# Kernel optimization log

Measured on AMD Instinct MI355X. Metric: run time of the kernel, lower is better.

Reference implementation:

```python
import jax, jax.numpy as jnp
import numpy as np

FEAT_DIM = 32
RES = 256
N_GAUSS = 500000
KSIZE = 5
SIGMA = 1.0


def setup_inputs() -> dict:
    key = jax.random.key(0)
    k0, k1, k2, k3, k4 = jax.random.split(key, 5)
    plane_xy = jax.random.normal(k0, (1, FEAT_DIM, RES, RES), jnp.float32)
    plane_xz = jax.random.normal(k1, (1, FEAT_DIM, RES, RES), jnp.float32)
    plane_yz = jax.random.normal(k2, (1, FEAT_DIM, RES, RES), jnp.float32)
    ln_weight = jnp.ones((FEAT_DIM, RES, RES), jnp.float32)
    ln_bias = jnp.zeros((FEAT_DIM, RES, RES), jnp.float32)
    gaussian_features = jax.random.normal(k3, (N_GAUSS, 3 * FEAT_DIM), jnp.float32)
    gaussian_xyz = jax.random.uniform(k4, (N_GAUSS, 3), jnp.float32, -1.0, 1.0)
    return {"plane_xy": plane_xy, "plane_xz": plane_xz, "plane_yz": plane_yz,
            "ln_weight": ln_weight, "ln_bias": ln_bias,
            "gaussian_features": gaussian_features, "gaussian_xyz": gaussian_xyz}


def _gaussian_blur(x):
    # depthwise 5x5 gaussian blur, groups = channels
    c = x.shape[1]
    k = jnp.arange(-(KSIZE // 2), KSIZE // 2 + 1, dtype=jnp.float32)
    k = jnp.exp(-0.5 * (k / SIGMA) ** 2)
    k = k / k.sum()
    k2d = k[:, None] * k[None, :]                       # [5,5]
    kern = jnp.broadcast_to(k2d, (c, 1, KSIZE, KSIZE))  # OIHW, grouped
    return jax.lax.conv_general_dilated(
        x, kern, window_strides=(1, 1), padding="SAME",
        feature_group_count=c,
        dimension_numbers=("NCHW", "OIHW", "NCHW"))


def _update_plane(plane, idx, feats, ln_w, ln_b):
    # plane [1,C,H,W]; idx [N,2] float pixel coords (x,y); feats [N,C]
    _, C, H, W = plane.shape
    px, py = idx[:, 0], idx[:, 1]
    px0 = jnp.clip(jnp.floor(px).astype(jnp.int32), 0, W - 1)
    px1 = jnp.clip(jnp.floor(px).astype(jnp.int32) + 1, 0, W - 1)
    py0 = jnp.clip(jnp.floor(py).astype(jnp.int32), 0, H - 1)
    py1 = jnp.clip(jnp.floor(py).astype(jnp.int32) + 1, 0, H - 1)
    wx0 = jnp.clip(px1.astype(px.dtype) - px, 0.0, 1.0)
    wx1 = jnp.clip(px - px0.astype(px.dtype), 0.0, 1.0)
    wy0 = jnp.clip(py1.astype(py.dtype) - py, 0.0, 1.0)
    wy1 = jnp.clip(py - py0.astype(py.dtype), 0.0, 1.0)
    weights = jnp.stack([wx0 * wy0, wx0 * wy1, wx1 * wy0, wx1 * wy1], axis=-1)  # [N,4]
    iy = jnp.stack([py0, py1, py0, py1], axis=-1)  # [N,4]
    ix = jnp.stack([px0, px0, px1, px1], axis=-1)  # [N,4]
    lin = (iy * W + ix).reshape(-1)                # [N*4]
    wf = (feats[:, None, :] * weights[:, :, None]).reshape(-1, C)  # [N*4, C]
    acc = jnp.zeros((H * W, C), plane.dtype).at[lin].add(wf)       # scatter-add
    counts = jnp.zeros((H * W,), plane.dtype).at[lin].add(1.0)
    flat = plane.reshape(C, H * W)
    # straight-through: value = scattered features, grad flows identity to plane
    new = flat + jax.lax.stop_gradient(-flat) + acc.T
    new = new / (counts[None, :] + 1e-6)
    new = new.reshape(1, C, H, W)
    # LayerNorm over (C,H,W)
    mu = jnp.mean(new, axis=(1, 2, 3), keepdims=True)
    var = jnp.var(new, axis=(1, 2, 3), keepdims=True)
    new = (new - mu) / jnp.sqrt(var + 1e-5) * ln_w[None] + ln_b[None]
    new = _gaussian_blur(new)
    return new + plane


def reference(plane_xy, plane_xz, plane_yz, ln_weight, ln_bias,
              gaussian_features, gaussian_xyz):
    res = plane_xy.shape[-1]
    xyz01 = (gaussian_xyz + 1.0) / 2.0
    x = jnp.clip(xyz01[..., 0], 0.0, 0.999) * (res - 1)
    y = jnp.clip(xyz01[..., 1], 0.0, 0.999) * (res - 1)
    z = jnp.clip(xyz01[..., 2], 0.0, 0.999) * (res - 1)
    feats = gaussian_features.reshape(gaussian_xyz.shape[0], 3, -1)
    new_xy = _update_plane(plane_xy, jnp.stack([x, y], -1), feats[:, 0, :], ln_weight, ln_bias)
    new_xz = _update_plane(plane_xz, jnp.stack([x, z], -1), feats[:, 1, :], ln_weight, ln_bias)
    new_yz = _update_plane(plane_yz, jnp.stack([y, z], -1), feats[:, 2, :], ln_weight, ln_bias)
    return (new_xy, new_xz, new_yz)
```

## Files before the change

kernel.cpp:

```cpp
#include <hip/hip_runtime.h>
#include <hip/hip_bf16.h>

#define N_GAUSS 500000
#define NGP (N_GAUSS * 3)
#define FEAT 32
#define RES 256
#define HW (RES * RES)
#define PLANE_ELEMS (FEAT * HW)
#define NBINS (3 * HW)

typedef __hip_bfloat16 bf16;

__device__ __forceinline__ bool input_is_bf16(const void* lnw) {
  return ((const unsigned int*)lnw)[0] == 0x3F803F80u;
}

template <bool BF16>
__device__ __forceinline__ float ldin(const void* p, size_t i) {
  if constexpr (BF16)
    return __bfloat162float(((const bf16*)p)[i]);
  else
    return ((const float*)p)[i];
}

template <bool BF16>
__device__ __forceinline__ float2 ldin2(const void* p, size_t i) {
  if constexpr (BF16) {
    unsigned u = *(const unsigned*)((const bf16*)p + i);
    return make_float2(__uint_as_float(u << 16),
                       __uint_as_float(u & 0xFFFF0000u));
  } else {
    return *(const float2*)((const float*)p + i);
  }
}

template <bool BF16>
__device__ __forceinline__ void stout(void* p, size_t i, float v) {
  if constexpr (BF16)
    ((bf16*)p)[i] = __float2bfloat16(v);
  else
    ((float*)p)[i] = v;
}

template <bool BF16>
__device__ __forceinline__ void gpos(const void* xyz, int g, int p, float& px,
                                     float& py) {
  int dx = (p == 2) ? 1 : 0;
  int dy = (p == 0) ? 1 : 2;
  float vx = ldin<BF16>(xyz, 3 * g + dx);
  float vy = ldin<BF16>(xyz, 3 * g + dy);
  px = fminf(fmaxf((vx + 1.0f) * 0.5f, 0.0f), 0.999f) * (float)(RES - 1);
  py = fminf(fmaxf((vy + 1.0f) * 0.5f, 0.0f), 0.999f) * (float)(RES - 1);
}

template <bool BF16>
__device__ __forceinline__ void count_impl(const void* xyz,
                                           int* __restrict__ bincnt) {
  int t = blockIdx.x * 256 + threadIdx.x;
  if (t >= NGP) return;
  int g = t / 3;
  int p = t - g * 3;
  float px, py;
  gpos<BF16>(xyz, g, p, px, py);
  atomicAdd(&bincnt[(p << 16) + ((int)py << 8) + (int)px], 1);
}

__global__ __launch_bounds__(256) void count_kernel(const void* __restrict__ xyz,
                                                    const void* __restrict__ lnw,
                                                    int* __restrict__ bincnt) {
  if (input_is_bf16(lnw))
    count_impl<true>(xyz, bincnt);
  else
    count_impl<false>(xyz, bincnt);
}

__global__ __launch_bounds__(256) void scan1_kernel(const int* __restrict__ bincnt,
                                                    int* __restrict__ off,
                                                    int* __restrict__ bsum) {
  int tid = threadIdx.x;
  int4 v = ((const int4*)bincnt)[blockIdx.x * 256 + tid];
  int s = v.x + v.y + v.z + v.w;
  __shared__ int ls[256];
  ls[tid] = s;
  __syncthreads();
  for (int o = 1; o < 256; o <<= 1) {
    int t = 0;
    if (tid >= o) t = ls[tid - o];
    __syncthreads();
    ls[tid] += t;
    __syncthreads();
  }
  int excl = ls[tid] - s;
  int base = blockIdx.x * 1024 + tid * 4;
  off[base + 0] = excl;
  off[base + 1] = excl + v.x;
  off[base + 2] = excl + v.x + v.y;
  off[base + 3] = excl + v.x + v.y + v.z;
  if (tid == 255) bsum[blockIdx.x] = ls[255];
}

__global__ __launch_bounds__(256) void scan23_kernel(int* __restrict__ off,
                                                     const int* __restrict__ bsum) {
  __shared__ int ls[256];
  __shared__ int ex[192];
  int tid = threadIdx.x;
  int v = (tid < 192) ? bsum[tid] : 0;
  ls[tid] = v;
  __syncthreads();
  for (int o = 1; o < 256; o <<= 1) {
    int t = 0;
    if (tid >= o) t = ls[tid - o];
    __syncthreads();
    ls[tid] += t;
    __syncthreads();
  }
  if (tid < 192) ex[tid] = ls[tid] - v;
  __syncthreads();
  int i = blockIdx.x * 256 + tid;
  off[i] += ex[blockIdx.x >> 2];
}

template <bool BF16>
__device__ __forceinline__ void scatter_impl(const void* xyz,
                                             int* __restrict__ off,
                                             int* __restrict__ entries) {
  int t = blockIdx.x * 256 + threadIdx.x;
  if (t >= NGP) return;
  int g = t / 3;
  int p = t - g * 3;
  float px, py;
  gpos<BF16>(xyz, g, p, px, py);
  int slot = atomicAdd(&off[(p << 16) + ((int)py << 8) + (int)px], 1);
  entries[slot * 3 + 0] = __float_as_int(px);
  entries[slot * 3 + 1] = __float_as_int(py);
  entries[slot * 3 + 2] = t << 5;
}

__global__ __launch_bounds__(256) void scatter_kernel(
    const void* __restrict__ xyz, const void* __restrict__ lnw,
    int* __restrict__ off, int* __restrict__ entries) {
  if (input_is_bf16(lnw))
    scatter_impl<true>(xyz, off, entries);
  else
    scatter_impl<false>(xyz, off, entries);
}

template <bool BF16>
__device__ __forceinline__ void gather_impl(const int* __restrict__ off,
                                            const int* __restrict__ bincnt,
                                            const int* __restrict__ entries,
                                            const void* __restrict__ feats,
                                            float* __restrict__ nb,
                                            float* tile) {
  int wid = threadIdx.x >> 6;
  int lane = threadIdx.x & 63;
  int c = lane & 31;
  int sub = lane >> 5;
  int pid4 = (blockIdx.x * 4 + wid) * 4;
  int p = pid4 >> 16;
  int pix = pid4 & 65535;
  int y = pix >> 8;
  int x0 = pix & 255;
  float fyq = (float)y;
  float fx0f = (float)x0;

  int bxlo = max(x0 - 1, 0);
  int rbA = (p << 16) + ((y - 1) << 8);
  int rbB = (p << 16) + (y << 8);
  int sA = 0, eA = 0;
  if (y > 0) {
    int bA0 = rbA + bxlo;
    sA = off[bA0] - bincnt[bA0];
    eA = off[rbA + x0 + 3];
  }
  int bB0 = rbB + bxlo;
  int sB = off[bB0] - bincnt[bB0];
  int eB = off[rbB + x0 + 3];

  int s0 = 0, s1 = 0, s2 = 0, s3 = 0, s4 = 0;
  {
    int col;
    col = x0 - 1;
    if (col >= 0) {
      s0 = bincnt[rbB + col];
      if (y > 0) s0 += bincnt[rbA + col];
    }
    col = x0;
    s1 = bincnt[rbB + col];
    if (y > 0) s1 += bincnt[rbA + col];
    col = x0 + 1;
    s2 = bincnt[rbB + col];
    if (y > 0) s2 += bincnt[rbA + col];
    col = x0 + 2;
    s3 = bincnt[rbB + col];
    if (y > 0) s3 += bincnt[rbA + col];
    col = x0 + 3;
    s4 = bincnt[rbB + col];
    if (y > 0) s4 += bincnt[rbA + col];
  }
  int cnt0 = s0 + s1, cnt1 = s1 + s2, cnt2 = s2 + s3, cnt3 = s3 + s4;

  float a0 = 0.0f, a1 = 0.0f, a2 = 0.0f, a3 = 0.0f;
#pragma unroll 1
  for (int rr = 0; rr < 2; ++rr) {
    int start = rr ? sB : sA;
    int end = rr ? eB : eA;
#pragma unroll 1
    for (int base = start; base < end; base += 20) {
      int n = end - base;
      n = n > 20 ? 20 : n;
      int d = 0;
      if (lane < n * 3) d = entries[base * 3 + lane];
      int l = lane < 20 ? lane : 19;
      float epx = __int_as_float(__shfl(d, 3 * l + 0));
      float epy = __int_as_float(__shfl(d, 3 * l + 1));
      int fbp = __shfl(d, 3 * l + 2);
      float wy = 1.0f - fabsf(epy - fyq);
      float u = epx - fx0f;
      float w0p = fmaxf(1.0f - fabsf(u), 0.0f) * wy;
      float w1p = fmaxf(1.0f - fabsf(u - 1.0f), 0.0f) * wy;
      float w2p = fmaxf(1.0f - fabsf(u - 2.0f), 0.0f) * wy;
      float w3p = fmaxf(1.0f - fabsf(u - 3.0f), 0.0f) * wy;
#pragma unroll 1
      for (int k = 0; k < n; k += 2) {
        int idx = k + sub;
        int is = idx < n ? idx : 0;
        int fb = __shfl(fbp, is);
        float f = ldin<BF16>(feats, (size_t)fb + c);
        if (idx >= n) f = 0.0f;
        a0 = fmaf(__shfl(w0p, is), f, a0);
        a1 = fmaf(__shfl(w1p, is), f, a1);
        a2 = fmaf(__shfl(w2p, is), f, a2);
        a3 = fmaf(__shfl(w3p, is), f, a3);
      }
    }
  }
  a0 += __shfl_xor(a0, 32);
  a1 += __shfl_xor(a1, 32);
  a2 += __shfl_xor(a2, 32);
  a3 += __shfl_xor(a3, 32);
  if (sub == 0) {
    int lb = (wid << 2);
    tile[c * 17 + lb + 0] = a0 / ((float)cnt0 + 1e-6f);
    tile[c * 17 + lb + 1] = a1 / ((float)cnt1 + 1e-6f);
    tile[c * 17 + lb + 2] = a2 / ((float)cnt2 + 1e-6f);
    tile[c * 17 + lb + 3] = a3 / ((float)cnt3 + 1e-6f);
  }
  __syncthreads();
  int c2 = threadIdx.x >> 4;
  int lp = threadIdx.x & 15;
  int pix0 = (blockIdx.x << 4) & 65535;
  size_t b = ((size_t)p << 21) + pix0 + lp;
  nb[b + ((size_t)c2 << 16)] = tile[c2 * 17 + lp];
  nb[b + ((size_t)(c2 + 16) << 16)] = tile[(c2 + 16) * 17 + lp];
}

__global__ __launch_bounds__(256) void gather_kernel(
    const int* __restrict__ off, const int* __restrict__ bincnt,
    const int* __restrict__ entries, const void* __restrict__ feats,
    const void* __restrict__ lnw, float* __restrict__ nb) {
  __shared__ float tile[32 * 17];
  if (input_is_bf16(lnw))
    gather_impl<true>(off, bincnt, entries, feats, nb, tile);
  else
    gather_impl<false>(off, bincnt, entries, feats, nb, tile);
}

__global__ __launch_bounds__(256) void stats_kernel(const float* __restrict__ nb,
                                                    double* __restrict__ stats) {
  int b = blockIdx.x;
  int p = b >> 8;
  int blk = b & 255;
  const float4* nb4 = (const float4*)(nb + ((size_t)p << 21));
  int tid = threadIdx.x;
  float s = 0.0f, s2 = 0.0f;
#pragma unroll
  for (int k = 0; k < 8; ++k) {
    float4 v = nb4[blk * 2048 + k * 256 + tid];
    s += (v.x + v.y) + (v.z + v.w);
    s2 += (v.x * v.x + v.y * v.y) + (v.z * v.z + v.w * v.w);
  }
  __shared__ float ls[256];
  __shared__ float ls2[256];
  ls[tid] = s;
  ls2[tid] = s2;
  __syncthreads();
  for (int o = 128; o > 0; o >>= 1) {
    if (tid < o) {
      ls[tid] += ls[tid + o];
      ls2[tid] += ls2[tid + o];
    }
    __syncthreads();
  }
  if (tid == 0) {
    unsafeAtomicAdd(&stats[2 * p + 0], (double)ls[0]);
    unsafeAtomicAdd(&stats[2 * p + 1], (double)ls2[0]);
  }
}

template <bool BF16>
__device__ __forceinline__ void blur_impl(const float* __restrict__ nb,
                                          const double* __restrict__ stats,
                                          const void* __restrict__ lnw,
                                          const void* __restrict__ lnb,
                                          const void* __restrict__ pl,
                                          void* __restrict__ out,
                                          float (*sm)[36]) {
  int p = blockIdx.z >> 5;
  int c = blockIdx.z & 31;
  const float* np = nb + ((size_t)p << 21) + ((size_t)c << 16);

  double mu_d = stats[2 * p] * (1.0 / PLANE_ELEMS);
  double var_d = stats[2 * p + 1] * (1.0 / PLANE_ELEMS) - mu_d * mu_d;
  float mu = (float)mu_d;
  float inv = rsqrtf((float)var_d + 1e-5f);

  int tx = threadIdx.x, ty = threadIdx.y;
  int w0 = blockIdx.x * 32, h0 = blockIdx.y * 8;
  int lid = ty * 32 + tx;
  for (int li = lid; li < 12 * 18; li += 256) {
    int r = li / 18;
    int m = li - r * 18;
    int hh = h0 - 2 + r;
    int ww = w0 - 2 + (m << 1);
    float v0 = 0.0f, v1 = 0.0f;
    if ((unsigned)hh < 256u && (unsigned)ww < 256u) {
      int pix = (hh << 8) + ww;
      float2 av = *(const float2*)(np + pix);
      size_t gi = ((size_t)c << 16) + pix;
      float2 lw = ldin2<BF16>(lnw, gi);
      float2 lb = ldin2<BF16>(lnb, gi);
      v0 = (av.x - mu) * inv * lw.x + lb.x;
      v1 = (av.y - mu) * inv * lw.y + lb.y;
    }
    sm[r][(m << 1) + 0] = v0;
    sm[r][(m << 1) + 1] = v1;
  }
  __syncthreads();

  const float K[5] = {0.054488685f, 0.24420134f, 0.40261996f, 0.24420134f,
                      0.054488685f};
  float a = 0.0f;
#pragma unroll
  for (int i = 0; i < 5; i++) {
    float rs = 0.0f;
#pragma unroll
    for (int j = 0; j < 5; j++) rs += K[j] * sm[ty + i][tx + j];
    a += K[i] * rs;
  }
  size_t idx = ((size_t)c << 16) + ((h0 + ty) << 8) + w0 + tx;
  float res = a + ldin<BF16>(pl, idx);
  stout<BF16>(out, ((size_t)p << 21) + idx, res);
}

__global__ __launch_bounds__(256) void blur_kernel(
    const float* __restrict__ nb, const double* __restrict__ stats,
    const void* __restrict__ lnw, const void* __restrict__ lnb,
    const void* __restrict__ p0, const void* __restrict__ p1,
    const void* __restrict__ p2, void* __restrict__ out) {
  __shared__ float sm[12][36];
  int p = blockIdx.z >> 5;
  const void* pl = (p == 0) ? p0 : ((p == 1) ? p1 : p2);
  if (input_is_bf16(lnw))
    blur_impl<true>(nb, stats, lnw, lnb, pl, out, sm);
  else
    blur_impl<false>(nb, stats, lnw, lnb, pl, out, sm);
}

extern "C" void kernel_launch(void* const* d_in, const int* in_sizes, int n_in,
                              void* d_out, int out_size, void* d_ws,
                              size_t ws_size, hipStream_t stream) {
  const void* plane_xy = d_in[0];
  const void* plane_xz = d_in[1];
  const void* plane_yz = d_in[2];
  const void* lnw = d_in[3];
  const void* lnb = d_in[4];
  const void* feats = d_in[5];
  const void* xyz = d_in[6];

  char* ws = (char*)d_ws;
  int* bincnt = (int*)ws;
  double* stats = (double*)(ws + 786432);
  int* off = (int*)(ws + 786480);
  int* bsum = (int*)(ws + 1572912);
  int* entries = (int*)(ws + 1574448);
  float* nb = (float*)(ws + 19574448);

  hipMemsetAsync(d_ws, 0, 786480, stream);

  int gp_blocks = (NGP + 255) / 256;
  count_kernel<<<gp_blocks, 256, 0, stream>>>(xyz, lnw, bincnt);
  scan1_kernel<<<192, 256, 0, stream>>>(bincnt, off, bsum);
  scan23_kernel<<<NBINS / 256, 256, 0, stream>>>(off, bsum);
  scatter_kernel<<<gp_blocks, 256, 0, stream>>>(xyz, lnw, off, entries);
  gather_kernel<<<NBINS / 16, 256, 0, stream>>>(off, bincnt, entries, feats,
                                                lnw, nb);
  stats_kernel<<<768, 256, 0, stream>>>(nb, stats);
  blur_kernel<<<dim3(8, 32, 96), dim3(32, 8), 0, stream>>>(
      nb, stats, lnw, lnb, plane_xy, plane_xz, plane_yz, d_out);
}
```

Measured before the change: 685.9 us.

## Process one gaussian per thread in count/scatter; prefetch entries and unroll gather loop

The count and scatter kernels now handle one gaussian per thread and cover all three planes, loading the xyz coordinates once instead of three times and dropping the divide-by-3. The gather kernel software-prefetches the next batch of 20 entries while it processes the current one, and fully unrolls the inner feature loop to 10 iterations with masking, so more feature loads can be in flight at once. The prefetch reads past the end of a bin's range, possibly past the end of the entries array, and may load garbage or out-of-bounds data. The unrolled loop also does wasted shuffles when a batch holds fewer than 20 entries.

Result: faster. 616.1 us (-10.2%).

```diff
diff --git a/kernel.cpp b/kernel.cpp
--- a/kernel.cpp
+++ b/kernel.cpp
@@ -42,27 +42,22 @@
     ((float*)p)[i] = v;
 }
 
-template <bool BF16>
-__device__ __forceinline__ void gpos(const void* xyz, int g, int p, float& px,
-                                     float& py) {
-  int dx = (p == 2) ? 1 : 0;
-  int dy = (p == 0) ? 1 : 2;
-  float vx = ldin<BF16>(xyz, 3 * g + dx);
-  float vy = ldin<BF16>(xyz, 3 * g + dy);
-  px = fminf(fmaxf((vx + 1.0f) * 0.5f, 0.0f), 0.999f) * (float)(RES - 1);
-  py = fminf(fmaxf((vy + 1.0f) * 0.5f, 0.0f), 0.999f) * (float)(RES - 1);
+__device__ __forceinline__ float gscale(float v) {
+  return fminf(fmaxf((v + 1.0f) * 0.5f, 0.0f), 0.999f) * (float)(RES - 1);
 }
 
 template <bool BF16>
 __device__ __forceinline__ void count_impl(const void* xyz,
                                            int* __restrict__ bincnt) {
-  int t = blockIdx.x * 256 + threadIdx.x;
-  if (t >= NGP) return;
-  int g = t / 3;
-  int p = t - g * 3;
-  float px, py;
-  gpos<BF16>(xyz, g, p, px, py);
-  atomicAdd(&bincnt[(p << 16) + ((int)py << 8) + (int)px], 1);
+  int g = blockIdx.x * 256 + threadIdx.x;
+  if (g >= N_GAUSS) return;
+  float s0 = gscale(ldin<BF16>(xyz, 3 * g + 0));
+  float s1 = gscale(ldin<BF16>(xyz, 3 * g + 1));
+  float s2 = gscale(ldin<BF16>(xyz, 3 * g + 2));
+  int i0 = (int)s0, i1 = (int)s1, i2 = (int)s2;
+  atomicAdd(&bincnt[(0 << 16) + (i1 << 8) + i0], 1);
+  atomicAdd(&bincnt[(1 << 16) + (i2 << 8) + i0], 1);
+  atomicAdd(&bincnt[(2 << 16) + (i2 << 8) + i1], 1);
 }
 
 __global__ __launch_bounds__(256) void count_kernel(const void* __restrict__ xyz,
@@ -124,16 +119,21 @@
 __device__ __forceinline__ void scatter_impl(const void* xyz,
                                              int* __restrict__ off,
                                              int* __restrict__ entries) {
-  int t = blockIdx.x * 256 + threadIdx.x;
-  if (t >= NGP) return;
-  int g = t / 3;
-  int p = t - g * 3;
-  float px, py;
-  gpos<BF16>(xyz, g, p, px, py);
-  int slot = atomicAdd(&off[(p << 16) + ((int)py << 8) + (int)px], 1);
-  entries[slot * 3 + 0] = __float_as_int(px);
-  entries[slot * 3 + 1] = __float_as_int(py);
-  entries[slot * 3 + 2] = t << 5;
+  int g = blockIdx.x * 256 + threadIdx.x;
+  if (g >= N_GAUSS) return;
+  float s0 = gscale(ldin<BF16>(xyz, 3 * g + 0));
+  float s1 = gscale(ldin<BF16>(xyz, 3 * g + 1));
+  float s2 = gscale(ldin<BF16>(xyz, 3 * g + 2));
+  float pxs[3] = {s0, s0, s1};
+  float pys[3] = {s1, s2, s2};
+#pragma unroll
+  for (int p = 0; p < 3; ++p) {
+    float px = pxs[p], py = pys[p];
+    int slot = atomicAdd(&off[(p << 16) + ((int)py << 8) + (int)px], 1);
+    entries[slot * 3 + 0] = __float_as_int(px);
+    entries[slot * 3 + 1] = __float_as_int(py);
+    entries[slot * 3 + 2] = (g * 3 + p) << 5;
+  }
 }
 
 __global__ __launch_bounds__(256) void scatter_kernel(
@@ -205,12 +205,13 @@
   for (int rr = 0; rr < 2; ++rr) {
     int start = rr ? sB : sA;
     int end = rr ? eB : eA;
+    if (start >= end) continue;
+    int d = entries[start * 3 + lane];
 #pragma unroll 1
     for (int base = start; base < end; base += 20) {
+      int dn = entries[(base + 20) * 3 + lane];
       int n = end - base;
       n = n > 20 ? 20 : n;
-      int d = 0;
-      if (lane < n * 3) d = entries[base * 3 + lane];
       int l = lane < 20 ? lane : 19;
       float epx = __int_as_float(__shfl(d, 3 * l + 0));
       float epy = __int_as_float(__shfl(d, 3 * l + 1));
@@ -221,9 +222,9 @@
       float w1p = fmaxf(1.0f - fabsf(u - 1.0f), 0.0f) * wy;
       float w2p = fmaxf(1.0f - fabsf(u - 2.0f), 0.0f) * wy;
       float w3p = fmaxf(1.0f - fabsf(u - 3.0f), 0.0f) * wy;
-#pragma unroll 1
-      for (int k = 0; k < n; k += 2) {
-        int idx = k + sub;
+#pragma unroll
+      for (int k = 0; k < 10; ++k) {
+        int idx = 2 * k + sub;
         int is = idx < n ? idx : 0;
         int fb = __shfl(fbp, is);
         float f = ldin<BF16>(feats, (size_t)fb + c);
@@ -233,6 +234,7 @@
         a2 = fmaf(__shfl(w2p, is), f, a2);
         a3 = fmaf(__shfl(w3p, is), f, a3);
       }
+      d = dn;
     }
   }
   a0 += __shfl_xor(a0, 32);
@@ -388,11 +390,11 @@
 
   hipMemsetAsync(d_ws, 0, 786480, stream);
 
-  int gp_blocks = (NGP + 255) / 256;
-  count_kernel<<<gp_blocks, 256, 0, stream>>>(xyz, lnw, bincnt);
+  int g_blocks = (N_GAUSS + 255) / 256;
+  count_kernel<<<g_blocks, 256, 0, stream>>>(xyz, lnw, bincnt);
   scan1_kernel<<<192, 256, 0, stream>>>(bincnt, off, bsum);
   scan23_kernel<<<NBINS / 256, 256, 0, stream>>>(off, bsum);
-  scatter_kernel<<<gp_blocks, 256, 0, stream>>>(xyz, lnw, off, entries);
+  scatter_kernel<<<g_blocks, 256, 0, stream>>>(xyz, lnw, off, entries);
   gather_kernel<<<NBINS / 16, 256, 0, stream>>>(off, bincnt, entries, feats,
                                                 lnw, nb);
   stats_kernel<<<768, 256, 0, stream>>>(nb, stats);
```
